# Kernel optimization log

Measured on AMD Instinct MI355X. Metric: run time of the kernel, lower is better.

Reference implementation:

```python
import jax, jax.numpy as jnp
import numpy as np

B, T, C_IN = 2, 4096, 1024
INTER, OUT = 1024, 1024
ROPE_DIM = 64
GAMMA = 0.99609375  # 1 - 2**-8
GROUPS = 32
EPS = 1e-6


def setup_inputs() -> dict:
    key = jax.random.key(0)
    k = jax.random.split(key, 4)
    return {
        "X_Q": jax.random.normal(k[0], (B, T, C_IN), dtype=jnp.float32),
        "W_Q": jax.random.normal(k[1], (C_IN, INTER), dtype=jnp.float32) / C_IN,
        "W_K": jax.random.normal(k[2], (C_IN, INTER), dtype=jnp.float32) / C_IN,
        "W_V": jax.random.normal(k[3], (C_IN, OUT), dtype=jnp.float32) / C_IN,
        "gn_weight": jnp.ones((OUT,), dtype=jnp.float32),
        "gn_bias": jnp.zeros((OUT,), dtype=jnp.float32),
    }


def _rope(x):
    # lucidrains RotaryEmbedding: rotate first ROPE_DIM features, pairwise-adjacent
    t = x.shape[-2]
    inv_freq = 1.0 / (10000.0 ** (jnp.arange(0, ROPE_DIM, 2, dtype=jnp.float32) / ROPE_DIM))
    freqs = jnp.arange(t, dtype=jnp.float32)[:, None] * inv_freq[None, :]  # [T, ROPE_DIM/2]
    freqs = jnp.repeat(freqs, 2, axis=-1)                                   # [T, ROPE_DIM]
    cos, sin = jnp.cos(freqs), jnp.sin(freqs)
    xr, xp = x[..., :ROPE_DIM], x[..., ROPE_DIM:]
    x1, x2 = xr[..., 0::2], xr[..., 1::2]
    rot = jnp.stack([-x2, x1], axis=-1).reshape(xr.shape)  # rotate_half (adjacent pairs)
    return jnp.concatenate([xr * cos + rot * sin, xp], axis=-1)


def _group_norm(x, w, b):
    # torch GroupNorm applied on x.reshape(-1, C)
    sh = x.shape
    c = sh[-1]
    xr = x.reshape(-1, GROUPS, c // GROUPS)
    mu = xr.mean(-1, keepdims=True)
    var = xr.var(-1, keepdims=True)
    xn = ((xr - mu) * jax.lax.rsqrt(var + EPS)).reshape(-1, c)
    return (xn * w + b).reshape(sh)


def reference(X_Q, W_Q, W_K, W_V, gn_weight, gn_bias):
    Q = jax.nn.silu(_rope(X_Q @ W_Q))  # [B,T,INTER]
    K = jax.nn.silu(_rope(X_Q @ W_K))
    V = jax.nn.silu(X_Q @ W_V)         # [B,T,OUT]
    A = jnp.einsum('btd,bsd->bts', Q, K)  # [B,T,T]
    # decay mask: original multiplies by _get_D(gamma,T).T -> gamma^(m-n) for m>=n
    n = jnp.arange(T)[:, None]
    m = jnp.arange(T)[None, :]
    upper = m >= n
    Dt = jnp.where(upper, GAMMA ** jnp.where(upper, m - n, 0).astype(jnp.float32), 0.0)
    A = A * Dt
    out = jnp.einsum('bts,bsd->btd', A, V)  # [B,T,OUT]
    # dropout p=0 (eval) -> identity
    return _group_norm(out, gn_weight, gn_bias)
```

## Files before the change

### kernel.cpp

```cpp
#include <hip/hip_runtime.h>


typedef __attribute__((ext_vector_type(8))) short bf16x8;
typedef __attribute__((ext_vector_type(4))) short bf16x4;
typedef __attribute__((ext_vector_type(4))) float f32x4;

#define MFMA16(a, b, c) __builtin_amdgcn_mfma_f32_16x16x32_bf16(a, b, c, 0, 0, 0)

static __device__ __forceinline__ short f2bf(float f) {
  unsigned u = __builtin_bit_cast(unsigned, f);
  u = (u + 0x7fffu + ((u >> 16) & 1u)) >> 16;
  return (short)u;
}

static __device__ __forceinline__ float fast_silu(float v) {
  return v * __builtin_amdgcn_rcpf(1.f + __expf(-v));
}

static __device__ __forceinline__ void gl_lds16(const void* g, void* l) {
  __builtin_amdgcn_global_load_lds(
      (const __attribute__((address_space(1))) void*)g,
      (__attribute__((address_space(3))) void*)l, 16, 0, 0);
}

static __device__ __forceinline__ int swzc(int col, int row) {
  return (((col >> 3) ^ (row & 7)) << 3) | (col & 7);
}

#define T_LEN 4096
#define CIN 1024

#define LOG2G (-0.0056465633f)
#define L2IF (0.41524101f)

__global__ __launch_bounds__(256)
void prep_kernel(const float* __restrict__ X, short* __restrict__ Xb,
                 const float* __restrict__ Wq, const float* __restrict__ Wk,
                 const float* __restrict__ Wv, short* __restrict__ WT) {
  __shared__ short tile[64][72];
  const int bx = blockIdx.x;
  const int tid = threadIdx.x;
  if (bx < 4096) {
    const int gid = bx * 256 + tid;
    const int row = gid >> 7;
    const int c = gid & 127;
    const float* s = &X[(size_t)gid * 8];
    float4 f0 = *(const float4*)s;
    float4 f1 = *(const float4*)(s + 4);
    bf16x8 v = {f2bf(f0.x), f2bf(f0.y), f2bf(f0.z), f2bf(f0.w),
                f2bf(f1.x), f2bf(f1.y), f2bf(f1.z), f2bf(f1.w)};
    const int pc = (c & 0x78) | ((c ^ row) & 7);
    *(bf16x8*)&Xb[(size_t)row * 1024 + pc * 8] = v;
    return;
  }
  const int bx2 = bx - 4096;
  const int k0 = (bx2 & 15) * 64, n0 = ((bx2 >> 4) & 15) * 64, mat = bx2 >> 8;
  const float* __restrict__ W = (mat == 0) ? Wq : (mat == 1) ? Wk : Wv;
  const int r = tid >> 4, c = tid & 15;
#pragma unroll
  for (int i = 0; i < 4; ++i) {
    int row = r + 16 * i;
    float4 f = *(const float4*)&W[(size_t)(k0 + row) * CIN + n0 + c * 4];
    tile[c * 4 + 0][row] = f2bf(f.x);
    tile[c * 4 + 1][row] = f2bf(f.y);
    tile[c * 4 + 2][row] = f2bf(f.z);
    tile[c * 4 + 3][row] = f2bf(f.w);
  }
  __syncthreads();
  const int n = tid >> 2, seg = tid & 3;
  bf16x8 lo = *(const bf16x8*)&tile[n][seg * 16];
  bf16x8 hi = *(const bf16x8*)&tile[n][seg * 16 + 8];
  const int R = mat * 1024 + n0 + n;
  const int a0 = (k0 >> 3) + seg * 2;
  short* base = &WT[(size_t)R * CIN];
  *(bf16x8*)&base[(a0 ^ (n & 7)) * 8] = lo;
  *(bf16x8*)&base[((a0 + 1) ^ (n & 7)) * 8] = hi;
}

#define GEMM_DECLS()                                   \
  const int tid = threadIdx.x;                         \
  const int lane = tid & 63, wave = tid >> 6;          \
  const int wm = wave >> 1, wn = wave & 1;             \
  const int l15 = lane & 15, quad = lane >> 4;         \
  const int srow = tid >> 3;                           \
  const int scol = (tid & 7) * 8;                      \
  const int asw = (l15 & 7);

#define ACC_INIT4(acc)                                 \
  _Pragma("unroll") for (int i = 0; i < 4; ++i)        \
  _Pragma("unroll") for (int j = 0; j < 4; ++j) {      \
    f32x4 z = {0.f, 0.f, 0.f, 0.f};                    \
    acc[i][j] = z;                                     \
  }

#define STAGE_TILE(dst, src, ld, r0, k0, nrows)        \
  _Pragma("unroll") for (int i = 0; i < (nrows) / 32; ++i) \
    gl_lds16(&src[(size_t)((r0) + i * 32 + srow) * (ld) + (k0) + scol], \
             &dst[i * 32 + srow][scol]);

#define FRAG_MFMA44(As, Bs, acc)                                            \
  {                                                                         \
    bf16x8 af[4][2], bfr[4][2];                                             \
    _Pragma("unroll") for (int im = 0; im < 4; ++im)                        \
    _Pragma("unroll") for (int ks = 0; ks < 2; ++ks)                        \
      af[im][ks] = *(const bf16x8*)&As[wm * 64 + im * 16 + l15]             \
                       [((ks * 4 + quad) ^ asw) * 8];                       \
    _Pragma("unroll") for (int in = 0; in < 4; ++in)                        \
    _Pragma("unroll") for (int ks = 0; ks < 2; ++ks)                        \
      bfr[in][ks] = *(const bf16x8*)&Bs[wn * 64 + in * 16 + l15]            \
                        [((ks * 4 + quad) ^ asw) * 8];                      \
    _Pragma("unroll") for (int ks = 0; ks < 2; ++ks)                        \
    _Pragma("unroll") for (int im = 0; im < 4; ++im)                        \
    _Pragma("unroll") for (int in = 0; in < 4; ++in)                        \
      acc[im][in] = MFMA16(af[im][ks], bfr[in][ks], acc[im][in]);           \
  }

__global__ __launch_bounds__(512, 4)
void qkv_gemm(const short* __restrict__ Xb, const short* __restrict__ WT,
              short* __restrict__ Qb, short* __restrict__ Kb,
              short* __restrict__ Vt) {
  __shared__ __align__(16) short As[256][64];
  __shared__ __align__(16) short Bs[128][64];
  GEMM_DECLS();
  const int m0 = blockIdx.x * 256;
  const int c0 = blockIdx.y * 128;

  f32x4 acc[4][4];
  ACC_INIT4(acc);

#pragma unroll 1
  for (int k0 = 0; k0 < CIN; k0 += 64) {
    __syncthreads();
#pragma unroll
    for (int i = 0; i < 4; ++i)
      gl_lds16(&Xb[(size_t)(m0 + i * 64 + srow) * CIN + k0 + scol],
               &As[i * 64 + srow][scol]);
#pragma unroll
    for (int i = 0; i < 2; ++i)
      gl_lds16(&WT[(size_t)(c0 + i * 64 + srow) * CIN + k0 + scol],
               &Bs[i * 64 + srow][scol]);
    __syncthreads();
    FRAG_MFMA44(As, Bs, acc);
  }

  const int mat = (c0 >> 10);
  const bool ropeBlk = (mat < 2) && ((c0 & 1023) == 0);
#pragma unroll
  for (int im = 0; im < 4; ++im) {
#pragma unroll
    for (int in = 0; in < 4; ++in) {
      const int c = c0 + wn * 64 + in * 16 + l15;
      const int colm = c & 1023;
      const int mbase = m0 + wm * 64 + im * 16 + quad * 4;
      short vv[4];
      if (ropeBlk && colm < 64) {
        const float invf = exp2f(-L2IF * (float)(colm >> 1));
#pragma unroll
        for (int r = 0; r < 4; ++r) {
          float v = acc[im][in][r];
          int t = (mbase + r) & (T_LEN - 1);
          float partner = __shfl_xor(v, 1, 64);
          float ang = (float)t * invf;
          float s_ = __sinf(ang), c_ = __cosf(ang);
          v = (colm & 1) ? (v * c_ + partner * s_) : (v * c_ - partner * s_);
          vv[r] = f2bf(fast_silu(v));
        }
      } else {
#pragma unroll
        for (int r = 0; r < 4; ++r) vv[r] = f2bf(fast_silu(acc[im][in][r]));
      }
      if (mat == 0) {
#pragma unroll
        for (int r = 0; r < 4; ++r)
          Qb[(size_t)(mbase + r) * 1024 + swzc(colm, mbase + r)] = vv[r];
      } else if (mat == 1) {
#pragma unroll
        for (int r = 0; r < 4; ++r)
          Kb[(size_t)(mbase + r) * 1024 + swzc(colm, mbase + r)] = vv[r];
      } else {
        bf16x4 v4 = {vv[0], vv[1], vv[2], vv[3]};
        *(bf16x4*)&Vt[(size_t)colm * 8192 +
                      (((mbase >> 3) ^ (colm & 7)) << 3) + (mbase & 7)] = v4;
      }
    }
  }
}

__global__ __launch_bounds__(512, 4)
void score_kernel(const short* __restrict__ Qb, const short* __restrict__ Kb,
                  short* __restrict__ Ab) {
  int idx = blockIdx.x;
  int ti = 0;
  while (idx >= 32 - 2 * ti) { idx -= 32 - 2 * ti; ++ti; }
  const int si = 2 * ti + idx;
  const int b = blockIdx.y;
  const int t0 = ti * 256, s0 = si * 128;

  __shared__ __align__(16) short Qs[256][64];
  __shared__ __align__(16) short Ks[128][64];
  GEMM_DECLS();

  f32x4 acc[4][4];
  ACC_INIT4(acc);

#pragma unroll 1
  for (int k0 = 0; k0 < 1024; k0 += 64) {
    __syncthreads();
#pragma unroll
    for (int i = 0; i < 4; ++i)
      gl_lds16(&Qb[(size_t)(b * T_LEN + t0 + i * 64 + srow) * 1024 + k0 + scol],
               &Qs[i * 64 + srow][scol]);
#pragma unroll
    for (int i = 0; i < 2; ++i)
      gl_lds16(&Kb[(size_t)(b * T_LEN + s0 + i * 64 + srow) * 1024 + k0 + scol],
               &Ks[i * 64 + srow][scol]);
    __syncthreads();
    FRAG_MFMA44(Qs, Ks, acc);
  }

#pragma unroll
  for (int im = 0; im < 4; ++im) {
#pragma unroll
    for (int in = 0; in < 4; ++in) {
      int s = s0 + wn * 64 + in * 16 + l15;
#pragma unroll
      for (int r = 0; r < 4; ++r) {
        int t = t0 + wm * 64 + im * 16 + quad * 4 + r;
        int d = s - t;
        float v = acc[im][in][r];
        v = (d < 0) ? 0.f : v * exp2f((float)d * LOG2G);
        Ab[((size_t)(b * T_LEN + t)) * T_LEN + swzc(s, t)] = f2bf(v);
      }
    }
  }
}

__global__ __launch_bounds__(256, 2)
void av_kernel(const short* __restrict__ Ab, const short* __restrict__ Vt,
               const float* __restrict__ gw, const float* __restrict__ gb,
               float* __restrict__ Out) {
  const int wgid = blockIdx.x;
  const int di = wgid & 7;
  const int q = (wgid >> 3) & 31;
  const int half = wgid >> 8;
  const int b = half;
  const int ti2 = half ? (31 - q) : q;
  const int t0 = ti2 * 128;
  const int n0 = di * 128;
  const int nIt = (T_LEN - t0) >> 6;

  __shared__ __align__(16) short As2[128][64];
  __shared__ __align__(16) short Vs[128][64];
  GEMM_DECLS();

  float w4[4], b4[4];
#pragma unroll
  for (int in = 0; in < 4; ++in) {
    int n = n0 + wn * 64 + in * 16 + l15;
    w4[in] = gw[n];
    b4[in] = gb[n];
  }

  f32x4 acc[4][4];
  ACC_INIT4(acc);

#pragma unroll 1
  for (int it = 0; it < nIt; ++it) {
    const int s = t0 + (it << 6);
    __syncthreads();
    STAGE_TILE(As2, Ab, T_LEN, b * T_LEN + t0, s, 128);
    STAGE_TILE(Vs, Vt, 8192, n0, b * T_LEN + s, 128);
    __syncthreads();
    FRAG_MFMA44(As2, Vs, acc);
  }

#pragma unroll
  for (int im = 0; im < 4; ++im) {
#pragma unroll
    for (int r = 0; r < 4; ++r) {
      int t = t0 + wm * 64 + im * 16 + quad * 4 + r;
      float* orow = &Out[((size_t)(b * T_LEN + t)) * 1024];
#pragma unroll
      for (int g = 0; g < 2; ++g) {
        float a0 = acc[im][g * 2][r], a1 = acc[im][g * 2 + 1][r];
        float s = a0 + a1;
        float qq = a0 * a0 + a1 * a1;
        s += __shfl_xor(s, 1, 64);
        qq += __shfl_xor(qq, 1, 64);
        s += __shfl_xor(s, 2, 64);
        qq += __shfl_xor(qq, 2, 64);
        s += __shfl_xor(s, 4, 64);
        qq += __shfl_xor(qq, 4, 64);
        s += __shfl_xor(s, 8, 64);
        qq += __shfl_xor(qq, 8, 64);
        float mean = s * (1.f / 32.f);
        float var = qq * (1.f / 32.f) - mean * mean;
        float rstd = rsqrtf(var + 1e-6f);
        int n = n0 + wn * 64 + g * 32 + l15;
        orow[n] = (a0 - mean) * rstd * w4[g * 2] + b4[g * 2];
        orow[n + 16] = (a1 - mean) * rstd * w4[g * 2 + 1] + b4[g * 2 + 1];
      }
    }
  }
}

extern "C" void kernel_launch(void* const* d_in, const int* in_sizes, int n_in,
                              void* d_out, int out_size, void* d_ws,
                              size_t ws_size, hipStream_t stream) {
  const float* X = (const float*)d_in[0];
  const float* Wq = (const float*)d_in[1];
  const float* Wk = (const float*)d_in[2];
  const float* Wv = (const float*)d_in[3];
  const float* gw = (const float*)d_in[4];
  const float* gb = (const float*)d_in[5];
  float* Out = (float*)d_out;

  short* Qb = (short*)d_ws;
  short* Kb = Qb + (size_t)8192 * 1024;
  short* Vt = Kb + (size_t)8192 * 1024;
  short* Ab = Vt + (size_t)8192 * 1024;
  short* Xb = Ab;
  short* WT = Xb + (size_t)8192 * 1024;

  prep_kernel<<<4864, 256, 0, stream>>>(X, Xb, Wq, Wk, Wv, WT);
  qkv_gemm<<<dim3(32, 24), 512, 0, stream>>>(Xb, WT, Qb, Kb, Vt);
  score_kernel<<<dim3(272, 2), 512, 0, stream>>>(Qb, Kb, Ab);
  av_kernel<<<512, 256, 0, stream>>>(Ab, Vt, gw, gb, Out);
}
```

Measured before the change: 291.3 us.

## Truncate decay band in score and AV kernels and retile AV to 256 rows

Result: faster. 265.7 us (-8.8%).

```diff
diff --git a/kernel.cpp b/kernel.cpp
--- a/kernel.cpp
+++ b/kernel.cpp
@@ -29,6 +29,8 @@
 
 #define T_LEN 4096
 #define CIN 1024
+#define AV_MAX_IT 36
+#define SC_MAX_SI 19
 
 #define LOG2G (-0.0056465633f)
 #define L2IF (0.41524101f)
@@ -191,7 +193,13 @@
                   short* __restrict__ Ab) {
   int idx = blockIdx.x;
   int ti = 0;
-  while (idx >= 32 - 2 * ti) { idx -= 32 - 2 * ti; ++ti; }
+  for (;;) {
+    int cnt = 32 - 2 * ti;
+    if (cnt > SC_MAX_SI) cnt = SC_MAX_SI;
+    if (idx < cnt) break;
+    idx -= cnt;
+    ++ti;
+  }
   const int si = 2 * ti + idx;
   const int b = blockIdx.y;
   const int t0 = ti * 256, s0 = si * 128;
@@ -235,21 +243,19 @@
   }
 }
 
-__global__ __launch_bounds__(256, 2)
+__global__ __launch_bounds__(512, 4)
 void av_kernel(const short* __restrict__ Ab, const short* __restrict__ Vt,
                const float* __restrict__ gw, const float* __restrict__ gb,
                float* __restrict__ Out) {
-  const int wgid = blockIdx.x;
-  const int di = wgid & 7;
-  const int q = (wgid >> 3) & 31;
-  const int half = wgid >> 8;
-  const int b = half;
-  const int ti2 = half ? (31 - q) : q;
-  const int t0 = ti2 * 128;
+  const int di = blockIdx.x;
+  const int ti = blockIdx.y;
+  const int b = blockIdx.z;
+  const int t0 = ti * 256;
   const int n0 = di * 128;
-  const int nIt = (T_LEN - t0) >> 6;
-
-  __shared__ __align__(16) short As2[128][64];
+  int nIt = (T_LEN - t0) >> 6;
+  if (nIt > AV_MAX_IT) nIt = AV_MAX_IT;
+
+  __shared__ __align__(16) short As2[256][64];
   __shared__ __align__(16) short Vs[128][64];
   GEMM_DECLS();
 
@@ -268,8 +274,14 @@
   for (int it = 0; it < nIt; ++it) {
     const int s = t0 + (it << 6);
     __syncthreads();
-    STAGE_TILE(As2, Ab, T_LEN, b * T_LEN + t0, s, 128);
-    STAGE_TILE(Vs, Vt, 8192, n0, b * T_LEN + s, 128);
+#pragma unroll
+    for (int i = 0; i < 4; ++i)
+      gl_lds16(&Ab[(size_t)(b * T_LEN + t0 + i * 64 + srow) * T_LEN + s + scol],
+               &As2[i * 64 + srow][scol]);
+#pragma unroll
+    for (int i = 0; i < 2; ++i)
+      gl_lds16(&Vt[(size_t)(n0 + i * 64 + srow) * 8192 + b * T_LEN + s + scol],
+               &Vs[i * 64 + srow][scol]);
     __syncthreads();
     FRAG_MFMA44(As2, Vs, acc);
   }
@@ -324,6 +336,6 @@
 
   prep_kernel<<<4864, 256, 0, stream>>>(X, Xb, Wq, Wk, Wv, WT);
   qkv_gemm<<<dim3(32, 24), 512, 0, stream>>>(Xb, WT, Qb, Kb, Vt);
-  score_kernel<<<dim3(272, 2), 512, 0, stream>>>(Qb, Kb, Ab);
-  av_kernel<<<512, 256, 0, stream>>>(Ab, Vt, gw, gb, Out);
-}
+  score_kernel<<<dim3(223, 2), 512, 0, stream>>>(Qb, Kb, Ab);
+  av_kernel<<<dim3(8, 16, 2), 512, 0, stream>>>(Ab, Vt, gw, gb, Out);
+}
```
